# Performance work log

Measured on AMD Instinct MI355X. Metric: run time of the kernel, lower is better.

## Reference

```python
import jax, jax.numpy as jnp
import numpy as np

E = 512   # embed_dim
H = 16    # num_heads
D = E // H  # head_dim = 32
L = 2048  # target (query) length
S = 2048  # source (stored pattern) length
N = 4     # batch
LN_EPS = 1e-5


def setup_inputs() -> dict:
    key = jax.random.key(0)
    ks = jax.random.split(key, 8)
    inv_sqrt_e = 1.0 / np.sqrt(E).astype(np.float32)
    return {
        "query": jax.random.normal(ks[0], (L, N, E), jnp.float32),
        "key_in": jax.random.normal(ks[1], (S, N, E), jnp.float32),
        "value": jax.random.normal(ks[2], (S, N, E), jnp.float32),
        "scaling": jax.random.uniform(ks[3], (H,), jnp.float32),  # per-head beta
        "in_proj_weight": jax.random.normal(ks[4], (3 * E, E), jnp.float32) * inv_sqrt_e,
        "in_proj_bias": jnp.zeros((3 * E,), jnp.float32),
        "p_norm_weight": jnp.ones((D,), jnp.float32),
        "p_norm_bias": jnp.zeros((D,), jnp.float32),
        "out_proj_weight": jax.random.normal(ks[5], (E, E), jnp.float32) * inv_sqrt_e,
        "out_proj_bias": jnp.zeros((E,), jnp.float32),
    }


def reference(query, key_in, value, scaling, in_proj_weight, in_proj_bias,
              p_norm_weight, p_norm_bias, out_proj_weight, out_proj_bias):
    Lq, Nb, Ed = query.shape
    Sk = key_in.shape[0]
    # split packed in-projection (torch Linear convention: y = x @ W^T + b)
    wq, wk, wv = jnp.split(in_proj_weight, 3, axis=0)
    bq, bk, bv = jnp.split(in_proj_bias, 3, axis=0)
    q = jnp.einsum('lne,fe->lnf', query, wq) + bq
    k = jnp.einsum('sne,fe->snf', key_in, wk) + bk
    v = jnp.einsum('sne,fe->snf', value, wv) + bv
    # (len, N, H*D) -> (N, H, len, D)
    q = q.reshape(Lq, Nb, H, D).transpose(1, 2, 0, 3)
    k = k.reshape(Sk, Nb, H, D).transpose(1, 2, 0, 3)
    v = v.reshape(Sk, Nb, H, D).transpose(1, 2, 0, 3)

    def pattern_norm(x):
        # affine LayerNorm over the association (head) dimension D
        mu = jnp.mean(x, axis=-1, keepdims=True)
        var = jnp.mean(jnp.square(x - mu), axis=-1, keepdims=True)
        return (x - mu) * jax.lax.rsqrt(var + LN_EPS) * p_norm_weight + p_norm_bias

    k = pattern_norm(k)
    v = pattern_norm(v)

    beta = scaling.reshape(1, H, 1, 1)  # per-head inverse-temperature
    scores = jnp.einsum('nhld,nhsd->nhls', q * beta, k)  # [N,H,L,S]
    attn = jax.nn.softmax(scores, axis=-1)  # single Hopfield update (update_steps_max=0)
    out = jnp.einsum('nhls,nhsd->nhld', attn, v)  # [N,H,L,D]
    out = out.transpose(2, 0, 1, 3).reshape(Lq, Nb, H * D)
    out = jnp.einsum('lnf,of->lno', out, out_proj_weight) + out_proj_bias
    return out  # (L, N, E)
```

## Files before the change

kernel.cpp:

```cpp
#include <hip/hip_runtime.h>
#include <cstdint>

#define LN_EPS 1e-5f

typedef _Float16 f16;
typedef _Float16 half4_t __attribute__((ext_vector_type(4)));
typedef _Float16 half8_t __attribute__((ext_vector_type(8)));
typedef __fp16 fp16v2 __attribute__((ext_vector_type(2)));
typedef float f32x4 __attribute__((ext_vector_type(4)));

__device__ __forceinline__ void gl_lds16(const void* g, void* l) {
    __builtin_amdgcn_global_load_lds(
        (__attribute__((address_space(1))) void*)(uintptr_t)g,
        (__attribute__((address_space(3))) void*)(uint32_t)(uintptr_t)l,
        16, 0, 0);
}

__device__ __forceinline__ half4_t pack4(float a, float b, float c, float d) {
    fp16v2 lo = __builtin_amdgcn_cvt_pkrtz(a, b);
    fp16v2 hi = __builtin_amdgcn_cvt_pkrtz(c, d);
    half4_t r;
    r[0] = (f16)lo[0]; r[1] = (f16)lo[1]; r[2] = (f16)hi[0]; r[3] = (f16)hi[1];
    return r;
}

__global__ void k_cast(const float* __restrict__ W1f, const float* __restrict__ W2f,
                       f16* __restrict__ W1h, f16* __restrict__ W2h) {
    int t = blockIdx.x * blockDim.x + threadIdx.x;
    const int n1 = (1536 * 512) / 4;
    const float4* src;
    half4_t* dst;
    int idx;
    if (t < n1) { src = (const float4*)W1f; dst = (half4_t*)W1h; idx = t; }
    else        { src = (const float4*)W2f; dst = (half4_t*)W2h; idx = t - n1; }
    float4 v = src[idx];
    dst[idx] = pack4(v.x, v.y, v.z, v.w);
}

__global__ __launch_bounds__(256) void k_inproj(
    const float* __restrict__ Xq, const float* __restrict__ Xk, const float* __restrict__ Xv,
    const f16* __restrict__ W1, const float* __restrict__ bias,
    const float* __restrict__ scaling,
    f16* __restrict__ Qg, f16* __restrict__ Kg, f16* __restrict__ Vg)
{
    __shared__ __align__(16) f16 Al[128 * 32];
    __shared__ __align__(16) f16 Bl[128 * 32];

    const int tid = threadIdx.x;
    const int m0 = blockIdx.x * 128;
    const int f0 = blockIdx.y * 128;
    const int sec = f0 >> 9;
    const float* X = (sec == 0) ? Xq : ((sec == 1) ? Xk : Xv);
    f16* Ob = (sec == 0) ? Qg : ((sec == 1) ? Kg : Vg);
    const int fl0 = f0 & 511;

    const int wid = tid >> 6, ln = tid & 63, l15 = ln & 15, quad = ln >> 4;
    const int wm = wid >> 1, wn = wid & 1;

    f32x4 z4 = {0.f, 0.f, 0.f, 0.f};
    f32x4 acc[4][4];
    #pragma unroll
    for (int i = 0; i < 4; ++i)
        #pragma unroll
        for (int j = 0; j < 4; ++j) acc[i][j] = z4;

    for (int kt = 0; kt < 16; ++kt) {
        const int k0 = kt * 32;
        #pragma unroll
        for (int i = 0; i < 2; ++i) {
            int row = wid * 32 + i * 16 + (ln >> 2);
            gl_lds16(W1 + (size_t)(f0 + row) * 512 + k0 + (ln & 3) * 8,
                     Bl + (wid * 32 + i * 16) * 32);
        }
        #pragma unroll
        for (int c = 0; c < 4; ++c) {
            int ch = c * 256 + tid;
            int row = ch >> 3, q4 = ch & 7;
            float4 v = *(const float4*)(X + (size_t)(m0 + row) * 512 + k0 + q4 * 4);
            *(half4_t*)(Al + row * 32 + q4 * 4) = pack4(v.x, v.y, v.z, v.w);
        }
        __syncthreads();

        half8_t a[4], b[4];
        #pragma unroll
        for (int i = 0; i < 4; ++i)
            a[i] = *(const half8_t*)(Al + (wm * 64 + i * 16 + l15) * 32 + quad * 8);
        #pragma unroll
        for (int j = 0; j < 4; ++j)
            b[j] = *(const half8_t*)(Bl + (wn * 64 + j * 16 + l15) * 32 + quad * 8);
        #pragma unroll
        for (int i = 0; i < 4; ++i)
            #pragma unroll
            for (int j = 0; j < 4; ++j)
                acc[i][j] = __builtin_amdgcn_mfma_f32_16x16x32_f16(b[j], a[i], acc[i][j], 0, 0, 0);
        __syncthreads();
    }

    #pragma unroll
    for (int j = 0; j < 4; ++j) {
        int fb = f0 + wn * 64 + j * 16;
        int floc = (fb & 511) + quad * 4;
        int hh = floc >> 5;
        int cc = (floc >> 3) & 3, e0 = floc & 7;
        float sc2 = (sec == 0) ? scaling[hh] * 1.44269504f : 1.0f;
        float4 bs4 = *(const float4*)(bias + fb + quad * 4);
        #pragma unroll
        for (int i = 0; i < 4; ++i) {
            int rm = m0 + wm * 64 + i * 16 + l15;
            int l = rm >> 2, nb = rm & 3;
            int gg = nb * 16 + hh;
            *(half4_t*)(Ob + (size_t)gg * 65536 + (size_t)cc * 16384 + (size_t)l * 8 + e0) =
                pack4((acc[i][j][0] + bs4.x) * sc2, (acc[i][j][1] + bs4.y) * sc2,
                      (acc[i][j][2] + bs4.z) * sc2, (acc[i][j][3] + bs4.w) * sc2);
        }
    }
}

__global__ void k_norm_k(f16* __restrict__ Kg, const float* __restrict__ w,
                         const float* __restrict__ b) {
    int t = blockIdx.x * 256 + threadIdx.x;
    int g = t >> 11, s = t & 2047;
    f16* base = Kg + (size_t)g * 65536 + (size_t)s * 8;
    half8_t x[4];
    float xf[32], s1 = 0.f, s2 = 0.f;
    #pragma unroll
    for (int c = 0; c < 4; ++c) {
        x[c] = *(const half8_t*)(base + (size_t)c * 16384);
        #pragma unroll
        for (int j = 0; j < 8; ++j) {
            float v = (float)x[c][j];
            xf[c * 8 + j] = v; s1 += v; s2 += v * v;
        }
    }
    float mean = s1 * (1.f / 32.f);
    float var = s2 * (1.f / 32.f) - mean * mean;
    float rs = rsqrtf(var + LN_EPS);
    #pragma unroll
    for (int c = 0; c < 4; ++c) {
        half8_t y;
        #pragma unroll
        for (int j = 0; j < 8; ++j) {
            int d = c * 8 + j;
            y[j] = (f16)((xf[d] - mean) * rs * w[d] + b[d]);
        }
        *(half8_t*)(base + (size_t)c * 16384) = y;
    }
}

__global__ void k_norm_vt(const f16* __restrict__ Vg, const float* __restrict__ w,
                          const float* __restrict__ b, f16* __restrict__ Vtg) {
    __shared__ __align__(16) f16 T[32 * 64];
    const int t = threadIdx.x;
    const int seg = blockIdx.x, g = blockIdx.y;
    const int s_l = t >> 2, c = t & 3;
    half8_t v = *(const half8_t*)(Vg + (size_t)g * 65536 + (size_t)c * 16384 +
                                  (size_t)(seg * 64 + s_l) * 8);
    float xf[8], s1 = 0.f, s2 = 0.f;
    #pragma unroll
    for (int j = 0; j < 8; ++j) { xf[j] = (float)v[j]; s1 += xf[j]; s2 += xf[j] * xf[j]; }
    s1 += __shfl_xor(s1, 1); s1 += __shfl_xor(s1, 2);
    s2 += __shfl_xor(s2, 1); s2 += __shfl_xor(s2, 2);
    float mean = s1 * (1.f / 32.f);
    float var = s2 * (1.f / 32.f) - mean * mean;
    float rs = rsqrtf(var + LN_EPS);
    int cs = s_l >> 3, es = s_l & 7;
    #pragma unroll
    for (int j = 0; j < 8; ++j) {
        int d = c * 8 + j;
        T[d * 64 + (cs ^ j) * 8 + es] = (f16)((xf[j] - mean) * rs * w[d] + b[d]);
    }
    __syncthreads();
    int d_o = t >> 3, c_o = t & 7;
    half8_t out = *(const half8_t*)(T + d_o * 64 + c_o * 8);
    *(half8_t*)(Vtg + (size_t)(g * 32 + seg) * 2048 + d_o * 64 + c_o * 8) = out;
}

__global__ __launch_bounds__(256, 6) void k_flash(
    const f16* __restrict__ Qg, const f16* __restrict__ Kg,
    const f16* __restrict__ Vtg, f16* __restrict__ Og)
{
    __shared__ __align__(16) char smem[25600];

    const int tid = threadIdx.x, wid = tid >> 6, ln = tid & 63;
    const int l15 = ln & 15, quad = ln >> 4;
    char* Pw = smem + 16384 + wid * 2304;
    const int g = blockIdx.y, h = g & 15, n = g >> 4;
    const int q0 = blockIdx.x * 64;

    gl_lds16(Qg + (size_t)g * 65536 + (size_t)wid * 16384 + (size_t)(q0 + ln) * 8,
             smem + 16384 + wid * 1024);
    gl_lds16(Kg + (size_t)g * 65536 + (size_t)wid * 16384 + (size_t)ln * 8,
             smem + wid * 1024);
    gl_lds16(Vtg + (size_t)(g * 32 + 0) * 2048 + wid * 512 + ln * 8,
             smem + 8192 + wid * 1024);
    __builtin_amdgcn_s_waitcnt(0x0F70);
    __syncthreads();
    half8_t aq = *(const half8_t*)(smem + 16384 + quad * 1024 + (wid * 16 + l15) * 16);

    f32x4 z4 = {0.f, 0.f, 0.f, 0.f};
    f32x4 accO[2];
    accO[0] = z4; accO[1] = z4;
    float m_i = -1e30f, l_i = 0.f;

    for (int st = 0; st < 32; ++st) {
        const int cur = st & 1, nxt = cur ^ 1;
        if (st < 31) {
            gl_lds16(Kg + (size_t)g * 65536 + (size_t)wid * 16384 + (size_t)((st + 1) * 64 + ln) * 8,
                     smem + nxt * 4096 + wid * 1024);
            gl_lds16(Vtg + (size_t)(g * 32 + st + 1) * 2048 + wid * 512 + ln * 8,
                     smem + 8192 + nxt * 4096 + wid * 1024);
        }
        const char* Kl = smem + cur * 4096;
        const char* Vt = smem + 8192 + cur * 4096;

        half8_t ak[4];
        #pragma unroll
        for (int mt = 0; mt < 4; ++mt)
            ak[mt] = *(const half8_t*)(Kl + quad * 1024 + (mt * 16 + l15) * 16);
        f32x4 accS[4];
        #pragma unroll
        for (int mt = 0; mt < 4; ++mt)
            accS[mt] = __builtin_amdgcn_mfma_f32_16x16x32_f16(ak[mt], aq, z4, 0, 0, 0);

        float xmax = accS[0][0];
        #pragma unroll
        for (int mt = 0; mt < 4; ++mt)
            #pragma unroll
            for (int r = 0; r < 4; ++r) xmax = fmaxf(xmax, accS[mt][r]);
        xmax = fmaxf(xmax, __shfl_xor(xmax, 16));
        xmax = fmaxf(xmax, __shfl_xor(xmax, 32));
        float mnew = fmaxf(m_i, xmax);
        float alpha = __builtin_amdgcn_exp2f(m_i - mnew);
        float rs = 0.f;
        #pragma unroll
        for (int mt = 0; mt < 4; ++mt) {
            float p0 = __builtin_amdgcn_exp2f(accS[mt][0] - mnew);
            float p1 = __builtin_amdgcn_exp2f(accS[mt][1] - mnew);
            float p2 = __builtin_amdgcn_exp2f(accS[mt][2] - mnew);
            float p3 = __builtin_amdgcn_exp2f(accS[mt][3] - mnew);
            rs += (p0 + p1) + (p2 + p3);
            *(half4_t*)(Pw + l15 * 144 + mt * 32 + quad * 8) = pack4(p0, p1, p2, p3);
        }
        rs += __shfl_xor(rs, 16);
        rs += __shfl_xor(rs, 32);
        l_i = l_i * alpha + rs;
        m_i = mnew;
        #pragma unroll
        for (int dt = 0; dt < 2; ++dt)
            #pragma unroll
            for (int r = 0; r < 4; ++r) accO[dt][r] *= alpha;

        #pragma unroll
        for (int kt = 0; kt < 2; ++kt) {
            half8_t av[2], bp;
            #pragma unroll
            for (int dt = 0; dt < 2; ++dt) {
                int d = dt * 16 + l15;
                int cp = (kt * 4 + quad) ^ (l15 & 7);
                av[dt] = *(const half8_t*)(Vt + d * 128 + cp * 16);
            }
            bp = *(const half8_t*)(Pw + l15 * 144 + kt * 64 + quad * 16);
            #pragma unroll
            for (int dt = 0; dt < 2; ++dt)
                accO[dt] = __builtin_amdgcn_mfma_f32_16x16x32_f16(av[dt], bp, accO[dt], 0, 0, 0);
        }

        __builtin_amdgcn_s_waitcnt(0x0F70);
        __syncthreads();
    }

    float inv = 1.f / l_i;
    #pragma unroll
    for (int dt = 0; dt < 2; ++dt)
        *(half4_t*)(Pw + l15 * 80 + (dt * 16 + quad * 4) * 2) =
            pack4(accO[dt][0] * inv, accO[dt][1] * inv,
                  accO[dt][2] * inv, accO[dt][3] * inv);
    int q2 = ln >> 2, c4 = ln & 3;
    half8_t o = *(const half8_t*)(Pw + q2 * 80 + c4 * 16);
    *(half8_t*)(Og + ((size_t)(n * 2048 + q0 + wid * 16 + q2)) * 512 + h * 32 + c4 * 8) = o;
}

__global__ __launch_bounds__(256) void k_outproj(
    const f16* __restrict__ A, const f16* __restrict__ W2,
    const float* __restrict__ bias, float* __restrict__ Out)
{
    __shared__ __align__(16) f16 Al[128 * 32];
    __shared__ __align__(16) f16 Bl[128 * 32];

    const int tid = threadIdx.x;
    const int m0 = blockIdx.x * 128;
    const int f0 = blockIdx.y * 128;
    const int wid = tid >> 6, ln = tid & 63, l15 = ln & 15, quad = ln >> 4;
    const int wm = wid >> 1, wn = wid & 1;

    f32x4 z4 = {0.f, 0.f, 0.f, 0.f};
    f32x4 acc[4][4];
    #pragma unroll
    for (int i = 0; i < 4; ++i)
        #pragma unroll
        for (int j = 0; j < 4; ++j) acc[i][j] = z4;

    for (int kt = 0; kt < 16; ++kt) {
        const int k0 = kt * 32;
        #pragma unroll
        for (int i = 0; i < 2; ++i) {
            int row = wid * 32 + i * 16 + (ln >> 2);
            gl_lds16(A + (size_t)(m0 + row) * 512 + k0 + (ln & 3) * 8,
                     Al + (wid * 32 + i * 16) * 32);
            gl_lds16(W2 + (size_t)(f0 + row) * 512 + k0 + (ln & 3) * 8,
                     Bl + (wid * 32 + i * 16) * 32);
        }
        __syncthreads();

        half8_t a[4], b[4];
        #pragma unroll
        for (int i = 0; i < 4; ++i)
            a[i] = *(const half8_t*)(Al + (wm * 64 + i * 16 + l15) * 32 + quad * 8);
        #pragma unroll
        for (int j = 0; j < 4; ++j)
            b[j] = *(const half8_t*)(Bl + (wn * 64 + j * 16 + l15) * 32 + quad * 8);
        #pragma unroll
        for (int i = 0; i < 4; ++i)
            #pragma unroll
            for (int j = 0; j < 4; ++j)
                acc[i][j] = __builtin_amdgcn_mfma_f32_16x16x32_f16(b[j], a[i], acc[i][j], 0, 0, 0);
        __syncthreads();
    }

    #pragma unroll
    for (int j = 0; j < 4; ++j) {
        int fb = f0 + wn * 64 + j * 16;
        float4 bs4 = *(const float4*)(bias + fb + quad * 4);
        #pragma unroll
        for (int i = 0; i < 4; ++i) {
            int rm = m0 + wm * 64 + i * 16 + l15;
            int orow = (rm & 2047) * 4 + (rm >> 11);
            float4 o;
            o.x = acc[i][j][0] + bs4.x;
            o.y = acc[i][j][1] + bs4.y;
            o.z = acc[i][j][2] + bs4.z;
            o.w = acc[i][j][3] + bs4.w;
            *(float4*)(Out + (size_t)orow * 512 + fb + quad * 4) = o;
        }
    }
}

extern "C" void kernel_launch(void* const* d_in, const int* in_sizes, int n_in,
                              void* d_out, int out_size, void* d_ws, size_t ws_size,
                              hipStream_t stream) {
    const float* query   = (const float*)d_in[0];
    const float* key_in  = (const float*)d_in[1];
    const float* value   = (const float*)d_in[2];
    const float* scaling = (const float*)d_in[3];
    const float* ipw     = (const float*)d_in[4];
    const float* ipb     = (const float*)d_in[5];
    const float* pnw     = (const float*)d_in[6];
    const float* pnb     = (const float*)d_in[7];
    const float* opw     = (const float*)d_in[8];
    const float* opb     = (const float*)d_in[9];
    float* out = (float*)d_out;

    f16* Qg  = (f16*)d_ws;
    f16* Kg  = Qg  + (size_t)4194304;
    f16* Vg  = Kg  + (size_t)4194304;
    f16* Vtg = Vg  + (size_t)4194304;
    f16* W1  = Vtg + (size_t)4194304;
    f16* W2  = W1  + (size_t)786432;
    f16* Og  = Vg;

    k_cast<<<1024, 256, 0, stream>>>(ipw, opw, W1, W2);
    k_inproj<<<dim3(64, 12), 256, 0, stream>>>(query, key_in, value, W1, ipb, scaling, Qg, Kg, Vg);
    k_norm_k<<<512, 256, 0, stream>>>(Kg, pnw, pnb);
    k_norm_vt<<<dim3(32, 64), 256, 0, stream>>>(Vg, pnw, pnb, Vtg);
    k_flash<<<dim3(32, 64), 256, 0, stream>>>(Qg, Kg, Vtg, Og);
    k_outproj<<<dim3(64, 4), 256, 0, stream>>>(Og, W2, opb, out);
}
```

Before: 245.5 us.

## Double query rows per flash warp, fuse K/V norms, compute row sums via MFMA

The flash kernel now handles 128 queries per block (32 per warp), so each K/V tile loaded into LDS is reused across twice as many query rows. The online-softmax rescale is skipped when no row max grows, and the row-sum reduction is replaced by an extra MFMA against a ones vector. The P buffer gets an XOR swizzle, and the separate K and V layernorm kernels are merged into one launch. This trades fewer blocks and lower occupancy (launch bounds 6 to 4) for fewer K/V loads and less shuffle and VALU work per query.

```diff
diff --git a/kernel.cpp b/kernel.cpp
--- a/kernel.cpp
+++ b/kernel.cpp
@@ -52,7 +52,6 @@
     const int sec = f0 >> 9;
     const float* X = (sec == 0) ? Xq : ((sec == 1) ? Xk : Xv);
     f16* Ob = (sec == 0) ? Qg : ((sec == 1) ? Kg : Vg);
-    const int fl0 = f0 & 511;
 
     const int wid = tid >> 6, ln = tid & 63, l15 = ln & 15, quad = ln >> 4;
     const int wm = wid >> 1, wn = wid & 1;
@@ -116,99 +115,97 @@
     }
 }
 
-__global__ void k_norm_k(f16* __restrict__ Kg, const float* __restrict__ w,
-                         const float* __restrict__ b) {
-    int t = blockIdx.x * 256 + threadIdx.x;
-    int g = t >> 11, s = t & 2047;
-    f16* base = Kg + (size_t)g * 65536 + (size_t)s * 8;
-    half8_t x[4];
-    float xf[32], s1 = 0.f, s2 = 0.f;
-    #pragma unroll
-    for (int c = 0; c < 4; ++c) {
-        x[c] = *(const half8_t*)(base + (size_t)c * 16384);
-        #pragma unroll
-        for (int j = 0; j < 8; ++j) {
-            float v = (float)x[c][j];
-            xf[c * 8 + j] = v; s1 += v; s2 += v * v;
-        }
-    }
-    float mean = s1 * (1.f / 32.f);
-    float var = s2 * (1.f / 32.f) - mean * mean;
-    float rs = rsqrtf(var + LN_EPS);
-    #pragma unroll
-    for (int c = 0; c < 4; ++c) {
-        half8_t y;
-        #pragma unroll
-        for (int j = 0; j < 8; ++j) {
-            int d = c * 8 + j;
-            y[j] = (f16)((xf[d] - mean) * rs * w[d] + b[d]);
-        }
-        *(half8_t*)(base + (size_t)c * 16384) = y;
-    }
-}
-
-__global__ void k_norm_vt(const f16* __restrict__ Vg, const float* __restrict__ w,
-                          const float* __restrict__ b, f16* __restrict__ Vtg) {
+__global__ void k_norm_kv(f16* __restrict__ Kg, const f16* __restrict__ Vg,
+                          const float* __restrict__ w, const float* __restrict__ b,
+                          f16* __restrict__ Vtg) {
     __shared__ __align__(16) f16 T[32 * 64];
     const int t = threadIdx.x;
     const int seg = blockIdx.x, g = blockIdx.y;
     const int s_l = t >> 2, c = t & 3;
-    half8_t v = *(const half8_t*)(Vg + (size_t)g * 65536 + (size_t)c * 16384 +
-                                  (size_t)(seg * 64 + s_l) * 8);
-    float xf[8], s1 = 0.f, s2 = 0.f;
-    #pragma unroll
-    for (int j = 0; j < 8; ++j) { xf[j] = (float)v[j]; s1 += xf[j]; s2 += xf[j] * xf[j]; }
-    s1 += __shfl_xor(s1, 1); s1 += __shfl_xor(s1, 2);
-    s2 += __shfl_xor(s2, 1); s2 += __shfl_xor(s2, 2);
-    float mean = s1 * (1.f / 32.f);
-    float var = s2 * (1.f / 32.f) - mean * mean;
-    float rs = rsqrtf(var + LN_EPS);
+    const size_t base = (size_t)g * 65536 + (size_t)c * 16384 + (size_t)(seg * 64 + s_l) * 8;
+
+    half8_t kv = *(const half8_t*)(Kg + base);
+    half8_t vv = *(const half8_t*)(Vg + base);
+    float kf[8], vf[8];
+    float ks1 = 0.f, ks2 = 0.f, vs1 = 0.f, vs2 = 0.f;
+    #pragma unroll
+    for (int j = 0; j < 8; ++j) {
+        kf[j] = (float)kv[j]; ks1 += kf[j]; ks2 += kf[j] * kf[j];
+        vf[j] = (float)vv[j]; vs1 += vf[j]; vs2 += vf[j] * vf[j];
+    }
+    ks1 += __shfl_xor(ks1, 1); ks1 += __shfl_xor(ks1, 2);
+    ks2 += __shfl_xor(ks2, 1); ks2 += __shfl_xor(ks2, 2);
+    vs1 += __shfl_xor(vs1, 1); vs1 += __shfl_xor(vs1, 2);
+    vs2 += __shfl_xor(vs2, 1); vs2 += __shfl_xor(vs2, 2);
+    float kmu = ks1 * (1.f / 32.f), kvar = ks2 * (1.f / 32.f) - kmu * kmu;
+    float vmu = vs1 * (1.f / 32.f), vvar = vs2 * (1.f / 32.f) - vmu * vmu;
+    float krs = rsqrtf(kvar + LN_EPS), vrs = rsqrtf(vvar + LN_EPS);
+
+    half8_t ky;
     int cs = s_l >> 3, es = s_l & 7;
     #pragma unroll
     for (int j = 0; j < 8; ++j) {
         int d = c * 8 + j;
-        T[d * 64 + (cs ^ j) * 8 + es] = (f16)((xf[j] - mean) * rs * w[d] + b[d]);
-    }
+        float wd = w[d], bd = b[d];
+        ky[j] = (f16)((kf[j] - kmu) * krs * wd + bd);
+        T[d * 64 + (cs ^ j) * 8 + es] = (f16)((vf[j] - vmu) * vrs * wd + bd);
+    }
+    *(half8_t*)(Kg + base) = ky;
     __syncthreads();
     int d_o = t >> 3, c_o = t & 7;
     half8_t out = *(const half8_t*)(T + d_o * 64 + c_o * 8);
     *(half8_t*)(Vtg + (size_t)(g * 32 + seg) * 2048 + d_o * 64 + c_o * 8) = out;
 }
 
-__global__ __launch_bounds__(256, 6) void k_flash(
+__global__ __launch_bounds__(256, 4) void k_flash(
     const f16* __restrict__ Qg, const f16* __restrict__ Kg,
     const f16* __restrict__ Vtg, f16* __restrict__ Og)
 {
-    __shared__ __align__(16) char smem[25600];
+    __shared__ __align__(16) char smem[32768];
 
     const int tid = threadIdx.x, wid = tid >> 6, ln = tid & 63;
-    const int l15 = ln & 15, quad = ln >> 4;
-    char* Pw = smem + 16384 + wid * 2304;
+    const int l15 = ln & 15, quad = ln >> 4, l8 = ln & 7;
+    char* Pw = smem + 16384 + wid * 4096;
     const int g = blockIdx.y, h = g & 15, n = g >> 4;
-    const int q0 = blockIdx.x * 64;
-
-    gl_lds16(Qg + (size_t)g * 65536 + (size_t)wid * 16384 + (size_t)(q0 + ln) * 8,
-             smem + 16384 + wid * 1024);
-    gl_lds16(Kg + (size_t)g * 65536 + (size_t)wid * 16384 + (size_t)ln * 8,
-             smem + wid * 1024);
-    gl_lds16(Vtg + (size_t)(g * 32 + 0) * 2048 + wid * 512 + ln * 8,
-             smem + 8192 + wid * 1024);
+    const int q0 = blockIdx.x * 128;
+
+    const f16* Qb = Qg + (size_t)g * 65536 + (size_t)wid * 16384 + (size_t)q0 * 8;
+    gl_lds16(Qb + (size_t)ln * 8,        smem + 16384 + wid * 2048);
+    gl_lds16(Qb + (size_t)(64 + ln) * 8, smem + 16384 + wid * 2048 + 1024);
+    const f16* kp = Kg + (size_t)g * 65536 + (size_t)wid * 16384;
+    const f16* vp = Vtg + (size_t)(g * 32) * 2048 + wid * 512;
+    gl_lds16(kp + (size_t)ln * 8, smem + wid * 1024);
+    gl_lds16(vp + (size_t)ln * 8, smem + 8192 + wid * 1024);
+    kp += 512;
+    vp += 2048;
     __builtin_amdgcn_s_waitcnt(0x0F70);
     __syncthreads();
-    half8_t aq = *(const half8_t*)(smem + 16384 + quad * 1024 + (wid * 16 + l15) * 16);
+    half8_t aq[2];
+    #pragma unroll
+    for (int i = 0; i < 2; ++i)
+        aq[i] = *(const half8_t*)(smem + 16384 + quad * 2048 + (wid * 32 + i * 16 + l15) * 16);
+    __syncthreads();
+
+    half8_t onesf;
+    {
+        f16 o = (l15 == 0) ? (f16)1.0f : (f16)0.0f;
+        #pragma unroll
+        for (int j = 0; j < 8; ++j) onesf[j] = o;
+    }
 
     f32x4 z4 = {0.f, 0.f, 0.f, 0.f};
-    f32x4 accO[2];
-    accO[0] = z4; accO[1] = z4;
-    float m_i = -1e30f, l_i = 0.f;
+    f32x4 accO[2][2], accSum[2];
+    accO[0][0] = z4; accO[0][1] = z4; accO[1][0] = z4; accO[1][1] = z4;
+    accSum[0] = z4; accSum[1] = z4;
+    float m_i[2] = {-1e30f, -1e30f};
 
     for (int st = 0; st < 32; ++st) {
-        const int cur = st & 1, nxt = cur ^ 1;
+        const int cur = st & 1;
         if (st < 31) {
-            gl_lds16(Kg + (size_t)g * 65536 + (size_t)wid * 16384 + (size_t)((st + 1) * 64 + ln) * 8,
-                     smem + nxt * 4096 + wid * 1024);
-            gl_lds16(Vtg + (size_t)(g * 32 + st + 1) * 2048 + wid * 512 + ln * 8,
-                     smem + 8192 + nxt * 4096 + wid * 1024);
+            gl_lds16(kp + (size_t)ln * 8, smem + (cur ^ 1) * 4096 + wid * 1024);
+            gl_lds16(vp + (size_t)ln * 8, smem + 8192 + (cur ^ 1) * 4096 + wid * 1024);
+            kp += 512;
+            vp += 2048;
         }
         const char* Kl = smem + cur * 4096;
         const char* Vt = smem + 8192 + cur * 4096;
@@ -217,67 +214,98 @@
         #pragma unroll
         for (int mt = 0; mt < 4; ++mt)
             ak[mt] = *(const half8_t*)(Kl + quad * 1024 + (mt * 16 + l15) * 16);
-        f32x4 accS[4];
-        #pragma unroll
-        for (int mt = 0; mt < 4; ++mt)
-            accS[mt] = __builtin_amdgcn_mfma_f32_16x16x32_f16(ak[mt], aq, z4, 0, 0, 0);
-
-        float xmax = accS[0][0];
-        #pragma unroll
-        for (int mt = 0; mt < 4; ++mt)
-            #pragma unroll
-            for (int r = 0; r < 4; ++r) xmax = fmaxf(xmax, accS[mt][r]);
-        xmax = fmaxf(xmax, __shfl_xor(xmax, 16));
-        xmax = fmaxf(xmax, __shfl_xor(xmax, 32));
-        float mnew = fmaxf(m_i, xmax);
-        float alpha = __builtin_amdgcn_exp2f(m_i - mnew);
-        float rs = 0.f;
-        #pragma unroll
-        for (int mt = 0; mt < 4; ++mt) {
-            float p0 = __builtin_amdgcn_exp2f(accS[mt][0] - mnew);
-            float p1 = __builtin_amdgcn_exp2f(accS[mt][1] - mnew);
-            float p2 = __builtin_amdgcn_exp2f(accS[mt][2] - mnew);
-            float p3 = __builtin_amdgcn_exp2f(accS[mt][3] - mnew);
-            rs += (p0 + p1) + (p2 + p3);
-            *(half4_t*)(Pw + l15 * 144 + mt * 32 + quad * 8) = pack4(p0, p1, p2, p3);
-        }
-        rs += __shfl_xor(rs, 16);
-        rs += __shfl_xor(rs, 32);
-        l_i = l_i * alpha + rs;
-        m_i = mnew;
-        #pragma unroll
-        for (int dt = 0; dt < 2; ++dt)
-            #pragma unroll
-            for (int r = 0; r < 4; ++r) accO[dt][r] *= alpha;
+        f32x4 accS[2][4];
+        #pragma unroll
+        for (int i = 0; i < 2; ++i)
+            #pragma unroll
+            for (int mt = 0; mt < 4; ++mt)
+                accS[i][mt] = __builtin_amdgcn_mfma_f32_16x16x32_f16(ak[mt], aq[i], z4, 0, 0, 0);
+
+        float mn[2];
+        bool up = false;
+        #pragma unroll
+        for (int i = 0; i < 2; ++i) {
+            float xm = fmaxf(fmaxf(accS[i][0][0], accS[i][0][1]),
+                             fmaxf(accS[i][0][2], accS[i][0][3]));
+            #pragma unroll
+            for (int mt = 1; mt < 4; ++mt)
+                xm = fmaxf(xm, fmaxf(fmaxf(accS[i][mt][0], accS[i][mt][1]),
+                                     fmaxf(accS[i][mt][2], accS[i][mt][3])));
+            xm = fmaxf(xm, __shfl_xor(xm, 16));
+            xm = fmaxf(xm, __shfl_xor(xm, 32));
+            up = up || (xm > m_i[i]);
+            mn[i] = fmaxf(m_i[i], xm);
+        }
+        if (__ballot(up)) {
+            #pragma unroll
+            for (int i = 0; i < 2; ++i) {
+                float alpha = __builtin_amdgcn_exp2f(m_i[i] - mn[i]);
+                #pragma unroll
+                for (int dt = 0; dt < 2; ++dt)
+                    #pragma unroll
+                    for (int r = 0; r < 4; ++r) accO[i][dt][r] *= alpha;
+                #pragma unroll
+                for (int r = 0; r < 4; ++r) accSum[i][r] *= alpha;
+            }
+        }
+        m_i[0] = mn[0]; m_i[1] = mn[1];
+
+        #pragma unroll
+        for (int i = 0; i < 2; ++i) {
+            #pragma unroll
+            for (int mt = 0; mt < 4; ++mt) {
+                float p0 = __builtin_amdgcn_exp2f(accS[i][mt][0] - mn[i]);
+                float p1 = __builtin_amdgcn_exp2f(accS[i][mt][1] - mn[i]);
+                float p2 = __builtin_amdgcn_exp2f(accS[i][mt][2] - mn[i]);
+                float p3 = __builtin_amdgcn_exp2f(accS[i][mt][3] - mn[i]);
+                int ch = (mt * 2 + (quad >> 1)) ^ l8;
+                *(half4_t*)(Pw + (i * 16 + l15) * 128 + ch * 16 + (quad & 1) * 8) =
+                    pack4(p0, p1, p2, p3);
+            }
+        }
 
         #pragma unroll
         for (int kt = 0; kt < 2; ++kt) {
-            half8_t av[2], bp;
+            half8_t av[2], bp[2];
             #pragma unroll
             for (int dt = 0; dt < 2; ++dt) {
                 int d = dt * 16 + l15;
                 int cp = (kt * 4 + quad) ^ (l15 & 7);
                 av[dt] = *(const half8_t*)(Vt + d * 128 + cp * 16);
             }
-            bp = *(const half8_t*)(Pw + l15 * 144 + kt * 64 + quad * 16);
-            #pragma unroll
-            for (int dt = 0; dt < 2; ++dt)
-                accO[dt] = __builtin_amdgcn_mfma_f32_16x16x32_f16(av[dt], bp, accO[dt], 0, 0, 0);
+            #pragma unroll
+            for (int i = 0; i < 2; ++i)
+                bp[i] = *(const half8_t*)(Pw + (i * 16 + l15) * 128 +
+                                          (((kt * 4 + quad) ^ l8) * 16));
+            #pragma unroll
+            for (int i = 0; i < 2; ++i) {
+                #pragma unroll
+                for (int dt = 0; dt < 2; ++dt)
+                    accO[i][dt] = __builtin_amdgcn_mfma_f32_16x16x32_f16(av[dt], bp[i], accO[i][dt], 0, 0, 0);
+                accSum[i] = __builtin_amdgcn_mfma_f32_16x16x32_f16(onesf, bp[i], accSum[i], 0, 0, 0);
+            }
         }
 
         __builtin_amdgcn_s_waitcnt(0x0F70);
         __syncthreads();
     }
 
-    float inv = 1.f / l_i;
-    #pragma unroll
-    for (int dt = 0; dt < 2; ++dt)
-        *(half4_t*)(Pw + l15 * 80 + (dt * 16 + quad * 4) * 2) =
-            pack4(accO[dt][0] * inv, accO[dt][1] * inv,
-                  accO[dt][2] * inv, accO[dt][3] * inv);
-    int q2 = ln >> 2, c4 = ln & 3;
-    half8_t o = *(const half8_t*)(Pw + q2 * 80 + c4 * 16);
-    *(half8_t*)(Og + ((size_t)(n * 2048 + q0 + wid * 16 + q2)) * 512 + h * 32 + c4 * 8) = o;
+    #pragma unroll
+    for (int i = 0; i < 2; ++i) {
+        float li = __shfl(accSum[i][0], l15);
+        float inv = 1.f / li;
+        #pragma unroll
+        for (int dt = 0; dt < 2; ++dt)
+            *(half4_t*)(Pw + (i * 16 + l15) * 80 + (dt * 16 + quad * 4) * 2) =
+                pack4(accO[i][dt][0] * inv, accO[i][dt][1] * inv,
+                      accO[i][dt][2] * inv, accO[i][dt][3] * inv);
+    }
+    int q2 = ln >> 1, hf = ln & 1;
+    half8_t o0 = *(const half8_t*)(Pw + q2 * 80 + hf * 32);
+    half8_t o1 = *(const half8_t*)(Pw + q2 * 80 + hf * 32 + 16);
+    size_t rowe = ((size_t)(n * 2048 + q0 + wid * 32 + q2)) * 512 + h * 32 + hf * 16;
+    *(half8_t*)(Og + rowe) = o0;
+    *(half8_t*)(Og + rowe + 8) = o1;
 }
 
 __global__ __launch_bounds__(256) void k_outproj(
@@ -370,8 +398,7 @@
 
     k_cast<<<1024, 256, 0, stream>>>(ipw, opw, W1, W2);
     k_inproj<<<dim3(64, 12), 256, 0, stream>>>(query, key_in, value, W1, ipb, scaling, Qg, Kg, Vg);
-    k_norm_k<<<512, 256, 0, stream>>>(Kg, pnw, pnb);
-    k_norm_vt<<<dim3(32, 64), 256, 0, stream>>>(Vg, pnw, pnb, Vtg);
-    k_flash<<<dim3(32, 64), 256, 0, stream>>>(Qg, Kg, Vtg, Og);
+    k_norm_kv<<<dim3(32, 64), 256, 0, stream>>>(Kg, Vg, pnw, pnb, Vtg);
+    k_flash<<<dim3(16, 64), 256, 0, stream>>>(Qg, Kg, Vtg, Og);
     k_outproj<<<dim3(64, 4), 256, 0, stream>>>(Og, W2, opb, out);
 }
```

Result: faster. 231.0 us (-5.9%).
